# Kernel optimization log

Hardware: AMD Instinct MI355X
Metric: run time of the kernel (lower is better)

Reference implementation:

```python
import jax, jax.numpy as jnp
import numpy as np
from jax import lax

RATE = 2          # self.rate
KS = 3            # kernel_size for matching patches
FUSE_K = 3        # fuse_k
SCALE = 10.0      # softmax_scale
EPS = 1e-4        # NaN guard in l2 norm


def extract_patches(x, size=3, step=1):
    """ZeroPad2d(1) then unfold -> (B, L, C, size, size) with L = Ho*Wo."""
    B, C, H, W = x.shape
    p = lax.conv_general_dilated_patches(
        x, (size, size), (step, step), padding=((1, 1), (1, 1)))
    Ho, Wo = p.shape[2], p.shape[3]
    # feature dim ordering of patches is (C, kh, kw)
    p = p.reshape(B, C, size, size, Ho, Wo)
    return p.transpose(0, 4, 5, 1, 2, 3).reshape(B, Ho * Wo, C, size, size)


def fuse_conv(s):
    """Conv with identity eye(k) kernel, pad 1 (diagonal propagation)."""
    w = jnp.eye(FUSE_K, dtype=s.dtype).reshape(1, 1, FUSE_K, FUSE_K)
    return lax.conv_general_dilated(s, w, (1, 1), ((1, 1), (1, 1)))


def contextual_attention(foreground, background, mask):
    B, C, H, W = foreground.shape
    # raw patches used as deconv filters: (B, L, C, 2*rate, 2*rate)
    raw_w = extract_patches(background, size=2 * RATE, step=RATE)
    # nearest downsample by rate (F.interpolate nearest, scale 1/rate == stride slice)
    fg = foreground[:, :, ::RATE, ::RATE]
    bg = background[:, :, ::RATE, ::RATE]
    fh, fw = fg.shape[2], fg.shape[3]
    bh, bw = bg.shape[2], bg.shape[3]
    # matching patches: (B, L, C, 3, 3), L = bh*bw
    w = extract_patches(bg, KS, 1)
    # mask patches -> per-patch validity (code uses batch 0 of the mask only)
    m = mask[:, :, ::RATE, ::RATE]
    mp = extract_patches(m, KS, 1)[0]            # (L, 1, 3, 3)
    mm = jnp.mean(mp, axis=(1, 2, 3))            # (L,)
    eq = (mm == 0.0).astype(foreground.dtype)[None, :, None, None]  # (1, L, 1, 1)
    # cosine-normalized filters
    norm = jnp.sqrt(jnp.sum(w * w, axis=(2, 3, 4), keepdims=True))
    wn = w / jnp.maximum(norm, EPS)
    # per-batch dynamic conv: scores (B, L, fh, fw)
    def score(f, wi):
        return lax.conv_general_dilated(f[None], wi, (1, 1), ((1, 1), (1, 1)))[0]
    s = jax.vmap(score)(fg, wn)
    # fuse: two identity-kernel convs with raw reshapes (faithful to torch .view,
    # including the discarded second permute in the original code)
    s = s.reshape(B, 1, fh * fw, bh * bw)
    s = fuse_conv(s)
    s = s.reshape(B, fh, fw, bh, bw).transpose(0, 2, 1, 4, 3)
    s = s.reshape(B, 1, fh * fw, bh * bw)
    s = fuse_conv(s)
    s = s.reshape(B, bh * bw, fh, fw)  # raw row-major reinterpret, as torch .view does
    # masked scaled softmax over background-patch dim
    s = s * eq
    s = jax.nn.softmax(s * SCALE, axis=1) * eq
    # per-batch deconv with raw patches as filters (conv_transpose2d stride=rate, pad=1)
    def deconv(si, rwi):
        # torch conv_transpose2d(W:(L,C,4,4)) == dilated conv with flipped, swapped kernel
        wt = jnp.flip(rwi, axis=(-2, -1)).transpose(1, 0, 2, 3)  # (C, L, 4, 4)
        pad = 2 * RATE - 1 - 1  # k - 1 - padding = 2
        return lax.conv_general_dilated(
            si[None], wt, (1, 1), ((pad, pad), (pad, pad)),
            lhs_dilation=(RATE, RATE))[0]
    y = jax.vmap(deconv)(s, raw_w) / 4.0  # (B, C, H, W)
    return y


def setup_inputs() -> dict:
    key = jax.random.key(0)
    k1, k2, k3 = jax.random.split(key, 3)
    B, C, H, W = 8, 128, 64, 64
    foreground = jax.random.normal(k1, (B, C, H, W), jnp.float32)
    background = jax.random.normal(k2, (B, C, H, W), jnp.float32)
    mask = (jax.random.uniform(k3, (1, 1, H, W)) < 0.25).astype(jnp.float32)
    return {"foreground": foreground, "background": background, "mask": mask}


def reference(foreground, background, mask):
    return contextual_attention(foreground, background, mask)
```

## Files before the change

### kernel.cpp

```cpp
#include <hip/hip_runtime.h>

typedef _Float16 half8 __attribute__((ext_vector_type(8)));
typedef float f32x4 __attribute__((ext_vector_type(4)));
typedef unsigned short us8 __attribute__((ext_vector_type(8)));
typedef unsigned short ush;
typedef unsigned int uint32;

#define IMGB 295936u
#define WROW 8704u

#define OFF_FGH  0ull
#define OFF_BGH  2367488ull
#define OFF_BGL  4734976ull
#define OFF_BGT  7102464ull
#define OFF_RN   15491072ull
#define OFF_LIST 15589376ull
#define OFF_NACT 15593472ull
#define OFF_S0   15597568ull
#define OFF_S2   49152000ull
#define OFF_WGT2 82706432ull

static __device__ __forceinline__ ush f2h(float f) {
    union { _Float16 h; ush u; } c; c.h = (_Float16)f; return c.u;
}
static __device__ __forceinline__ float h2f(ush u) {
    union { _Float16 h; ush u; } c; c.u = u; return (float)c.h;
}
__device__ __forceinline__ int untr(int v) { return ((v & 31) << 5) | (v >> 5); }

__global__ void k_prep2(const float* __restrict__ fg, const float* __restrict__ bg,
                        ush* __restrict__ fgh3, ush* __restrict__ bgh,
                        ush* __restrict__ bgl, ush* __restrict__ BGt) {
    int y = blockIdx.x, b = blockIdx.y, t = threadIdx.x;
    __shared__ float lds[64 * 129];
    __shared__ float fls[32 * 129];
    int xx = t & 63;
    for (int c0 = 0; c0 < 128; c0 += 4) {
        int c = c0 + (t >> 6);
        lds[xx * 129 + c] = bg[((b * 128 + c) * 64 + y) * 64 + xx];
    }
    __syncthreads();
    uint32* dst = (uint32*)(BGt + (size_t)(b * 64 + y) * 8192);
    for (int j = t; j < 4096; j += 256) {
        int x = j >> 6, cp = (j & 63) * 2;
        uint32 h0 = f2h(lds[x * 129 + cp]);
        uint32 h1 = f2h(lds[x * 129 + cp + 1]);
        dst[j] = h0 | (h1 << 16);
    }
    if ((y & 1) != 0) return;
    int yd = y >> 1;
    {
        int xq = t & 31, cg = t >> 5;
        for (int c0 = 0; c0 < 128; c0 += 8) {
            int c = c0 + cg;
            fls[xq * 129 + c] = fg[((b * 128 + c) * 64 + y) * 64 + 2 * xq];
        }
    }
    __syncthreads();
    unsigned base = ((b * 34 + yd + 1) * 34 + 1) * 128;
    for (int k = t; k < 2048; k += 256) {
        int x = k >> 6, c = (k & 63) * 2;
        float vb0 = lds[(2 * x) * 129 + c], vb1 = lds[(2 * x) * 129 + c + 1];
        float vf0 = fls[x * 129 + c],       vf1 = fls[x * 129 + c + 1];
        _Float16 bh0 = (_Float16)vb0, bh1 = (_Float16)vb1;
        float br0 = vb0 - (float)bh0, br1 = vb1 - (float)bh1;
        union { _Float16 h; ush u; } x0, x1;
        x0.h = bh0; x1.h = bh1;
        uint32 b01 = (uint32)x0.u | ((uint32)x1.u << 16);
        uint32 l01 = (uint32)f2h(br0) | ((uint32)f2h(br1) << 16);
        ((uint32*)(bgh + base))[k] = b01;
        ((uint32*)(bgl + base))[k] = l01;
        uint32 f01 = (uint32)f2h(vf0) | ((uint32)f2h(vf1) << 16);
        int ch = c >> 6, g = (c >> 3) & 7, cl = c & 7;
        unsigned pix = (unsigned)(yd + 1) * 34 + (x + 1);
        unsigned ui = (((unsigned)(b * 16 + ch * 8 + g) * 1156 + pix) << 2) + (cl >> 1);
        ((uint32*)fgh3)[ui] = f01;
    }
    unsigned cb0 = ((unsigned)(b * 34 + yd + 1) * 34) * 64;
    if (t < 64) {
        ((uint32*)bgh)[cb0 + t] = 0; ((uint32*)bgl)[cb0 + t] = 0;
    } else if (t < 128) {
        unsigned cb1 = cb0 + 33 * 64 + (t - 64);
        ((uint32*)bgh)[cb1] = 0; ((uint32*)bgl)[cb1] = 0;
    } else if (t < 256) {
        int tt = t - 128;
        unsigned pix = (unsigned)(yd + 1) * 34 + ((tt >> 6) ? 33u : 0u);
        int pl = tt & 63, plane = pl >> 2, w = pl & 3;
        ((uint32*)fgh3)[(((unsigned)(b * 16 + plane) * 1156 + pix) << 2) + w] = 0;
    }
    if (yd == 0 || yd == 31) {
        int prow = (yd == 0) ? 0 : 33;
        unsigned rb = (unsigned)(b * 34 + prow) * 2176;
        for (int k = t; k < 2176; k += 256) {
            ((uint32*)bgh)[rb + k] = 0; ((uint32*)bgl)[rb + k] = 0;
            int plane = k / 136, rem = k - plane * 136;
            unsigned pix = (unsigned)prow * 34 + (rem >> 2);
            ((uint32*)fgh3)[(((unsigned)(b * 16 + plane) * 1156 + pix) << 2) + (rem & 3)] = 0;
        }
    }
}

__global__ void k_ssnq(const ush* __restrict__ bgh, const ush* __restrict__ bgl,
                       const float* __restrict__ mask, float* __restrict__ rnorm,
                       int* __restrict__ L, int* __restrict__ nact) {
    int bx = blockIdx.x, b = blockIdx.y, t = threadIdx.x;
    __shared__ float ssh[10][32];
    __shared__ int ps[256];
    if (bx == 4) {
        if (b != 0) return;
        int fl[4], s = 0;
#pragma unroll
        for (int j = 0; j < 4; ++j) {
            int l = t * 4 + j;
            int hm = l >> 5, wm = l & 31;
            int any = 0;
            for (int di = -1; di <= 1; ++di)
                for (int dj = -1; dj <= 1; ++dj) {
                    int yy = hm + di, xxx = wm + dj;
                    if (yy >= 0 && yy < 32 && xxx >= 0 && xxx < 32)
                        any |= (mask[(2 * yy) * 64 + 2 * xxx] != 0.0f);
                }
            fl[j] = !any; s += fl[j];
        }
        ps[t] = s;
        __syncthreads();
        for (int off = 1; off < 256; off <<= 1) {
            int v = (t >= off) ? ps[t - off] : 0;
            __syncthreads();
            ps[t] += v;
            __syncthreads();
        }
        int base = ps[t] - s;
#pragma unroll
        for (int j = 0; j < 4; ++j)
            if (fl[j]) L[base++] = t * 4 + j;
        if (t == 255) nact[0] = ps[255];
        return;
    }
    int r0 = bx * 8;
    for (int idx = t; idx < 320; idx += 256) {
        int row = idx >> 5, xx = idx & 31;
        int gy = r0 - 1 + row;
        float s = 0.f;
        if (gy >= 0 && gy < 32) {
            size_t base = ((size_t)(b * 34 + gy + 1) * 34 + xx + 1) * 128;
            for (int c = 0; c < 128; c += 8) {
                us8 vh = *(const us8*)(bgh + base + c);
                us8 vl = *(const us8*)(bgl + base + c);
#pragma unroll
                for (int j = 0; j < 8; ++j) {
                    float v = h2f(vh[j]) + h2f(vl[j]);
                    s += v * v;
                }
            }
        }
        ssh[row][xx] = s;
    }
    __syncthreads();
    int pr = t >> 5, pc = t & 31;
    float n2 = 0.f;
#pragma unroll
    for (int di = -1; di <= 1; ++di)
#pragma unroll
        for (int dj = -1; dj <= 1; ++dj) {
            int xx = pc + dj;
            if (xx >= 0 && xx < 32) n2 += ssh[pr + 1 + di][xx];
        }
    rnorm[b * 1024 + (r0 + pr) * 32 + pc] = 1.0f / fmaxf(sqrtf(n2), 1e-4f);
}

__global__ __launch_bounds__(256, 2)
void k_smfma(const ush* __restrict__ fgh3, const ush* __restrict__ bgh,
             const ush* __restrict__ bgl, const float* __restrict__ rnorm,
             float* __restrict__ s0) {
    int qt = blockIdx.x, pt = blockIdx.y, b = blockIdx.z;
    int t = threadIdx.x, wid = t >> 6, lane = t & 63;
    int wp = wid >> 1, wq = wid & 1;
    __shared__ ulong2 smem_raw[3328];
    char* smem = (char*)smem_raw;

    const char* base0 = (const char*)bgh + (size_t)b * IMGB + (unsigned)(pt * 4) * WROW;
    const char* base1 = (const char*)bgl + (size_t)b * IMGB + (unsigned)(pt * 4) * WROW;

    f32x4 acc[4][4];
#pragma unroll
    for (int i = 0; i < 4; ++i)
#pragma unroll
        for (int j = 0; j < 4; ++j) acc[i][j] = (f32x4){0.f, 0.f, 0.f, 0.f};

    int r15 = lane & 15, hi2 = lane >> 4;
    for (int ch = 0; ch < 2; ++ch) {
        __syncthreads();
        {
            int pixl = (lane >> 3);
            int sl = lane & 7;
            for (int idx = wid; idx < 52; idx += 4) {
                int a = idx / 26;
                int chunk = idx - a * 26;
                int pix = chunk * 8 + pixl;
                int g = sl ^ (pix & 7);
                const char* sb = a ? base1 : base0;
                const char* gp = sb + ((unsigned)pix << 8) + ((unsigned)ch << 7)
                               + ((unsigned)g << 4);
                char* lp = smem + (unsigned)(a * 26624 + chunk * 1024);
                __builtin_amdgcn_global_load_lds(
                    (const __attribute__((address_space(1))) void*)gp,
                    (__attribute__((address_space(3))) void*)lp, 16, 0, 0);
            }
        }
        __syncthreads();

        const char* Aimg = (const char*)fgh3
                         + (((size_t)(b * 16 + ch * 8)) * 1156 + (unsigned)(qt * 136)) * 16;
        for (int o = 0; o < 9; ++o) {
            int dy = o / 3, dx = o - 3 * (o / 3);
            int pixB[4], pixA[4];
#pragma unroll
            for (int i = 0; i < 4; ++i) {
                pixB[i] = (wp * 2 + (i >> 1) + dy) * 34 + (i & 1) * 16 + r15 + dx;
                pixA[i] = (wq * 2 + (i >> 1) + dy) * 34 + (i & 1) * 16 + r15 + dx;
            }
#pragma unroll
            for (int cc = 0; cc < 2; ++cc) {
                int g = cc * 4 + hi2;
                half8 bh[4], bl[4], af[4];
#pragma unroll
                for (int i = 0; i < 4; ++i) {
                    unsigned offB = ((unsigned)pixB[i] << 7) + ((unsigned)(g ^ (pixB[i] & 7)) << 4);
                    bh[i] = *(const half8*)(smem + offB);
                    bl[i] = *(const half8*)(smem + 26624 + offB);
                    af[i] = *(const half8*)(Aimg + (((size_t)g * 1156 + pixA[i]) << 4));
                }
#pragma unroll
                for (int i = 0; i < 4; ++i)
#pragma unroll
                    for (int j = 0; j < 4; ++j) {
                        acc[i][j] = __builtin_amdgcn_mfma_f32_16x16x32_f16(bh[i], af[j], acc[i][j], 0, 0, 0);
                        acc[i][j] = __builtin_amdgcn_mfma_f32_16x16x32_f16(bl[i], af[j], acc[i][j], 0, 0, 0);
                    }
            }
        }
    }
    int col = lane & 15, rgrp = (lane >> 4) << 2;
#pragma unroll
    for (int i = 0; i < 4; ++i) {
        int Pb = pt * 128 + wp * 64 + i * 16 + rgrp;
        float rn0 = rnorm[b * 1024 + Pb + 0];
        float rn1 = rnorm[b * 1024 + Pb + 1];
        float rn2 = rnorm[b * 1024 + Pb + 2];
        float rn3 = rnorm[b * 1024 + Pb + 3];
#pragma unroll
        for (int j = 0; j < 4; ++j) {
            int Q = qt * 128 + wq * 64 + j * 16 + col;
            float* dst = s0 + ((size_t)(b * 1024 + Pb) << 10) + Q;
            dst[0]    = acc[i][j][0] * rn0;
            dst[1024] = acc[i][j][1] * rn1;
            dst[2048] = acc[i][j][2] * rn2;
            dst[3072] = acc[i][j][3] * rn3;
        }
    }
}

__global__ void k_fuse(const float* __restrict__ s0, float* __restrict__ s2t,
                       const int* __restrict__ L, const int* __restrict__ nactp) {
    int nact = *nactp;
    int b = blockIdx.z;
    int u = blockIdx.x * 256 + threadIdx.x;
    int T = untr(u);
    const float* S = s0 + (size_t)b * 1048576;
    for (int ai = blockIdx.y; ai < nact; ai += 32) {
        int R = L[ai];
        float acc = 0.f;
#pragma unroll
        for (int k = -1; k <= 1; ++k) {
            int Rk = R + k, Tk = T + k;
            if ((unsigned)Rk < 1024u && (unsigned)Tk < 1024u) {
                int Pr = untr(Rk), Qc = untr(Tk);
#pragma unroll
                for (int j = -1; j <= 1; ++j) {
                    int r = Pr + j, cI = Qc + j;
                    if ((unsigned)r < 1024u && (unsigned)cI < 1024u)
                        acc += S[(size_t)r * 1024 + cI];
                }
            }
        }
        s2t[(size_t)b * 1048576 + (size_t)R * 1024 + u] = acc;
    }
}

__global__ __launch_bounds__(256)
void k_ctsw(const ush* __restrict__ BGt, const float* __restrict__ s2t,
            const int* __restrict__ L, const int* __restrict__ nactp,
            ush* __restrict__ CT, ush* __restrict__ W2) {
    int bx = blockIdx.x, b = blockIdx.y, t = threadIdx.x;
    int nact = *nactp;
    __shared__ float sm[32][8], sd[32][8];
    __shared__ float Msh[32], RDsh[32];
    __shared__ ush wt[32][136];
    if (bx < 16) {
        int KPAD = (nact + 31) & ~31;
        int ab = bx, a = ab >> 2, bb = ab & 3;
        for (int ai0 = 0; ai0 < KPAD; ai0 += 256) {
            int ai = ai0 + t;
            if (ai >= KPAD) break;
            int ok = 0;
            const ush* srow = nullptr;
            if (ai < nact) {
                int R = L[ai];
                int hb = R >> 5, wb = R & 31;
                int row = 2 * hb - 1 + a, col = 2 * wb - 1 + bb;
                if (row >= 0 && row < 64 && col >= 0 && col < 64) {
                    ok = 1;
                    srow = BGt + ((size_t)((b * 64 + row) * 64 + col) << 7);
                }
            }
            ush* dst = CT + ((size_t)(b * 16 + ab) << 15) + ai;
#pragma unroll 4
            for (int c = 0; c < 128; ++c)
                dst[(size_t)c << 8] = ok ? srow[c] : (ush)0;
        }
        return;
    }
    int uc = bx - 16;
    int u0 = uc * 32;
    int part = t >> 5, ul = t & 31;
    {
        const float* S = s2t + (size_t)b * 1048576 + u0 + ul;
        float m = -3e38f, d = 0.f;
        for (int ai = part; ai < nact; ai += 8) {
            float v = S[(size_t)L[ai] << 10];
            if (v > m) { d *= expf(10.f * (m - v)); m = v; }
            d += expf(10.f * (v - m));
        }
        sm[ul][part] = m; sd[ul][part] = d;
    }
    __syncthreads();
    if (t < 32) {
        float mm = -3e38f, dd = 0.f;
#pragma unroll
        for (int p = 0; p < 8; ++p) {
            float m2 = sm[t][p], d2 = sd[t][p];
            if (m2 > mm) { dd *= expf(10.f * (mm - m2)); mm = m2; dd += d2; }
            else dd += d2 * expf(10.f * (m2 - mm));
        }
        int cnt0 = 1024 - nact;
        if (cnt0 > 0) {
            if (mm < 0.f) { dd *= expf(10.f * mm); mm = 0.f; }
            dd += (float)cnt0 * expf(-10.f * mm);
        }
        Msh[t] = mm; RDsh[t] = 1.f / dd;
    }
    __syncthreads();
    for (int kp = 0; kp < 16; ++kp) {
        int k = kp * 8 + part;
        float w = 0.f;
        if (k < nact) {
            float v = s2t[((size_t)(b * 1024 + L[k]) << 10) + u0 + ul];
            w = expf(10.f * (v - Msh[ul])) * RDsh[ul];
        }
        wt[ul][k] = f2h(w);
    }
    __syncthreads();
    {
        int ur = t >> 3, kb = t & 7;
        int uu = u0 + ur;
        int p1 = (uu & 31) + 1, q1 = (uu >> 5) + 1;
        ush* dstr = W2 + (((size_t)(b * 35 + p1) * 35 + q1) << 7) + kb * 16;
        *(half8*)dstr       = *(const half8*)&wt[ur][kb * 16];
        *(half8*)(dstr + 8) = *(const half8*)&wt[ur][kb * 16 + 8];
    }
    for (int r = uc; r < 1225; r += 32) {
        int p1 = r / 35, q1 = r - p1 * 35;
        if (p1 < 1 || p1 > 32 || q1 < 1 || q1 > 32) {
            uint32* row = (uint32*)(W2 + (((size_t)(b * 35 + p1) * 35 + q1) << 7));
            if (t < 64) row[t] = 0;
        }
    }
}

__global__ __launch_bounds__(256, 4)
void k_dgemm(const ush* __restrict__ CT, const ush* __restrict__ W2,
             const int* __restrict__ nactp, float* __restrict__ y) {
    int nact = *nactp;
    int KPAD = (nact + 31) & ~31;
    int pt2 = blockIdx.x;
    int par = blockIdx.y, b = blockIdx.z;
    int a_lo = par >> 1, b_lo = par & 1;
    int P0 = 1 - a_lo, Q0 = 1 - b_lo;
    int p_lo = P0 + pt2;
    int wid = threadIdx.x >> 6, lane = threadIdx.x & 63;
    int r15 = lane & 15, kg = (lane >> 4) << 3;

    f32x4 acc[2][2];
#pragma unroll
    for (int i = 0; i < 2; ++i)
#pragma unroll
        for (int j = 0; j < 2; ++j) acc[i][j] = (f32x4){0.f, 0.f, 0.f, 0.f};

    for (int k0 = 0; k0 < KPAD; k0 += 32) {
#pragma unroll
        for (int pp = 0; pp < 2; ++pp)
#pragma unroll
            for (int qq = 0; qq < 2; ++qq) {
                int ab = (a_lo + 2 * pp) * 4 + (b_lo + 2 * qq);
                const ush* Ab = CT + ((size_t)(b * 16 + ab) << 15)
                              + ((unsigned)(wid * 32) << 8) + k0 + kg;
                int p1 = p_lo - pp + 1;
                int q1b = Q0 - qq + 1;
                const ush* Bb = W2 + (((size_t)(b * 35 + p1) * 35 + q1b) << 7) + k0 + kg;
                half8 A[2], B[2];
                A[0] = *(const half8*)(Ab + ((unsigned)r15 << 8));
                A[1] = *(const half8*)(Ab + ((unsigned)(16 + r15) << 8));
                B[0] = *(const half8*)(Bb + ((unsigned)r15 << 7));
                B[1] = *(const half8*)(Bb + ((unsigned)(16 + r15) << 7));
#pragma unroll
                for (int i = 0; i < 2; ++i)
#pragma unroll
                    for (int j = 0; j < 2; ++j)
                        acc[i][j] = __builtin_amdgcn_mfma_f32_16x16x32_f16(A[i], B[j], acc[i][j], 0, 0, 0);
            }
    }
    int col = r15, rgrp = (lane >> 4) << 2;
    int oy = 2 * p_lo + a_lo - 1;
#pragma unroll
    for (int i = 0; i < 2; ++i) {
        int c = wid * 32 + i * 16 + rgrp;
#pragma unroll
        for (int j = 0; j < 2; ++j) {
            int q_lo = Q0 + j * 16 + col;
            int ox = 2 * q_lo + b_lo - 1;
            float* Y = y + ((size_t)((b * 128 + c) * 64 + oy) << 6) + ox;
            Y[0]         = acc[i][j][0] * 0.25f;
            Y[4096]      = acc[i][j][1] * 0.25f;
            Y[2 * 4096]  = acc[i][j][2] * 0.25f;
            Y[3 * 4096]  = acc[i][j][3] * 0.25f;
        }
    }
}

extern "C" void kernel_launch(void* const* d_in, const int* in_sizes, int n_in,
                              void* d_out, int out_size, void* d_ws, size_t ws_size,
                              hipStream_t stream) {
    (void)in_sizes; (void)n_in; (void)out_size; (void)ws_size;
    const float* fg   = (const float*)d_in[0];
    const float* bg   = (const float*)d_in[1];
    const float* mask = (const float*)d_in[2];
    float* y = (float*)d_out;
    char* ws = (char*)d_ws;

    ush*   fgh3  = (ush*)(ws + OFF_FGH);
    ush*   bgh   = (ush*)(ws + OFF_BGH);
    ush*   bgl   = (ush*)(ws + OFF_BGL);
    ush*   BGt   = (ush*)(ws + OFF_BGT);
    float* rnorm = (float*)(ws + OFF_RN);
    int*   Lst   = (int*)(ws + OFF_LIST);
    int*   nact  = (int*)(ws + OFF_NACT);
    float* s0    = (float*)(ws + OFF_S0);
    ush*   CT    = (ush*)(ws + OFF_S0);
    float* s2t   = (float*)(ws + OFF_S2);
    ush*   W2    = (ush*)(ws + OFF_WGT2);

    k_prep2<<<dim3(64, 8), 256, 0, stream>>>(fg, bg, fgh3, bgh, bgl, BGt);
    k_ssnq<<<dim3(5, 8), 256, 0, stream>>>(bgh, bgl, mask, rnorm, Lst, nact);
    k_smfma<<<dim3(8, 8, 8), 256, 0, stream>>>(fgh3, bgh, bgl, rnorm, s0);
    k_fuse<<<dim3(4, 32, 8), 256, 0, stream>>>(s0, s2t, Lst, nact);
    k_ctsw<<<dim3(48, 8), 256, 0, stream>>>(BGt, s2t, Lst, nact, CT, W2);
    k_dgemm<<<dim3(32, 4, 8), 256, 0, stream>>>(CT, W2, nact, y);
}
```

Baseline: 116.3 us.

## Fold norm/mask kernel into prep and compute patch norms inside score GEMM

Removes the separate k_ssnq launch. The per-pixel channel sum of squares is now computed in k_prep2 from the fp32 background already staged in LDS, and an extra block handles the mask scan. k_smfma then builds each 3x3 patch's reciprocal norm from those sums into shared memory before its GEMM. This saves one kernel launch and a reread of the split-half background, at the cost of a little redundant stencil work per GEMM block. Norms now come from exact fp32 values instead of the hi+lo half reconstruction.

```diff
diff --git a/kernel.cpp b/kernel.cpp
--- a/kernel.cpp
+++ b/kernel.cpp
@@ -13,7 +13,7 @@
 #define OFF_BGH  2367488ull
 #define OFF_BGL  4734976ull
 #define OFF_BGT  7102464ull
-#define OFF_RN   15491072ull
+#define OFF_SS   15523840ull
 #define OFF_LIST 15589376ull
 #define OFF_NACT 15593472ull
 #define OFF_S0   15597568ull
@@ -29,11 +29,47 @@
 __device__ __forceinline__ int untr(int v) { return ((v & 31) << 5) | (v >> 5); }
 
 __global__ void k_prep2(const float* __restrict__ fg, const float* __restrict__ bg,
+                        const float* __restrict__ mask,
                         ush* __restrict__ fgh3, ush* __restrict__ bgh,
-                        ush* __restrict__ bgl, ush* __restrict__ BGt) {
+                        ush* __restrict__ bgl, ush* __restrict__ BGt,
+                        float* __restrict__ SS, int* __restrict__ L,
+                        int* __restrict__ nact) {
     int y = blockIdx.x, b = blockIdx.y, t = threadIdx.x;
     __shared__ float lds[64 * 129];
     __shared__ float fls[32 * 129];
+    __shared__ float sm2[32][8];
+    __shared__ int ps[256];
+    if (y == 64) {
+        if (b != 0) return;
+        int fl[4], s = 0;
+#pragma unroll
+        for (int j = 0; j < 4; ++j) {
+            int l = t * 4 + j;
+            int hm = l >> 5, wm = l & 31;
+            int any = 0;
+            for (int di = -1; di <= 1; ++di)
+                for (int dj = -1; dj <= 1; ++dj) {
+                    int yy = hm + di, xxx = wm + dj;
+                    if (yy >= 0 && yy < 32 && xxx >= 0 && xxx < 32)
+                        any |= (mask[(2 * yy) * 64 + 2 * xxx] != 0.0f);
+                }
+            fl[j] = !any; s += fl[j];
+        }
+        ps[t] = s;
+        __syncthreads();
+        for (int off = 1; off < 256; off <<= 1) {
+            int v = (t >= off) ? ps[t - off] : 0;
+            __syncthreads();
+            ps[t] += v;
+            __syncthreads();
+        }
+        int base = ps[t] - s;
+#pragma unroll
+        for (int j = 0; j < 4; ++j)
+            if (fl[j]) L[base++] = t * 4 + j;
+        if (t == 255) nact[0] = ps[255];
+        return;
+    }
     int xx = t & 63;
     for (int c0 = 0; c0 < 128; c0 += 4) {
         int c = c0 + (t >> 6);
@@ -56,7 +92,24 @@
             fls[xq * 129 + c] = fg[((b * 128 + c) * 64 + y) * 64 + 2 * xq];
         }
     }
+    {
+        int xd = t & 31, part = t >> 5;
+        float s = 0.f;
+        int c0 = part * 16;
+#pragma unroll
+        for (int c = 0; c < 16; ++c) {
+            float v = lds[(2 * xd) * 129 + c0 + c];
+            s += v * v;
+        }
+        sm2[xd][part] = s;
+    }
     __syncthreads();
+    if (t < 32) {
+        float s = 0.f;
+#pragma unroll
+        for (int p = 0; p < 8; ++p) s += sm2[t][p];
+        SS[b * 1024 + yd * 32 + t] = s;
+    }
     unsigned base = ((b * 34 + yd + 1) * 34 + 1) * 128;
     for (int k = t; k < 2048; k += 256) {
         int x = k >> 6, c = (k & 63) * 2;
@@ -100,84 +153,34 @@
     }
 }
 
-__global__ void k_ssnq(const ush* __restrict__ bgh, const ush* __restrict__ bgl,
-                       const float* __restrict__ mask, float* __restrict__ rnorm,
-                       int* __restrict__ L, int* __restrict__ nact) {
-    int bx = blockIdx.x, b = blockIdx.y, t = threadIdx.x;
-    __shared__ float ssh[10][32];
-    __shared__ int ps[256];
-    if (bx == 4) {
-        if (b != 0) return;
-        int fl[4], s = 0;
-#pragma unroll
-        for (int j = 0; j < 4; ++j) {
-            int l = t * 4 + j;
-            int hm = l >> 5, wm = l & 31;
-            int any = 0;
-            for (int di = -1; di <= 1; ++di)
-                for (int dj = -1; dj <= 1; ++dj) {
-                    int yy = hm + di, xxx = wm + dj;
-                    if (yy >= 0 && yy < 32 && xxx >= 0 && xxx < 32)
-                        any |= (mask[(2 * yy) * 64 + 2 * xxx] != 0.0f);
-                }
-            fl[j] = !any; s += fl[j];
-        }
-        ps[t] = s;
-        __syncthreads();
-        for (int off = 1; off < 256; off <<= 1) {
-            int v = (t >= off) ? ps[t - off] : 0;
-            __syncthreads();
-            ps[t] += v;
-            __syncthreads();
-        }
-        int base = ps[t] - s;
-#pragma unroll
-        for (int j = 0; j < 4; ++j)
-            if (fl[j]) L[base++] = t * 4 + j;
-        if (t == 255) nact[0] = ps[255];
-        return;
-    }
-    int r0 = bx * 8;
-    for (int idx = t; idx < 320; idx += 256) {
-        int row = idx >> 5, xx = idx & 31;
-        int gy = r0 - 1 + row;
-        float s = 0.f;
-        if (gy >= 0 && gy < 32) {
-            size_t base = ((size_t)(b * 34 + gy + 1) * 34 + xx + 1) * 128;
-            for (int c = 0; c < 128; c += 8) {
-                us8 vh = *(const us8*)(bgh + base + c);
-                us8 vl = *(const us8*)(bgl + base + c);
-#pragma unroll
-                for (int j = 0; j < 8; ++j) {
-                    float v = h2f(vh[j]) + h2f(vl[j]);
-                    s += v * v;
-                }
-            }
-        }
-        ssh[row][xx] = s;
-    }
-    __syncthreads();
-    int pr = t >> 5, pc = t & 31;
-    float n2 = 0.f;
-#pragma unroll
-    for (int di = -1; di <= 1; ++di)
-#pragma unroll
-        for (int dj = -1; dj <= 1; ++dj) {
-            int xx = pc + dj;
-            if (xx >= 0 && xx < 32) n2 += ssh[pr + 1 + di][xx];
-        }
-    rnorm[b * 1024 + (r0 + pr) * 32 + pc] = 1.0f / fmaxf(sqrtf(n2), 1e-4f);
-}
-
 __global__ __launch_bounds__(256, 2)
 void k_smfma(const ush* __restrict__ fgh3, const ush* __restrict__ bgh,
-             const ush* __restrict__ bgl, const float* __restrict__ rnorm,
+             const ush* __restrict__ bgl, const float* __restrict__ SS,
              float* __restrict__ s0) {
     int qt = blockIdx.x, pt = blockIdx.y, b = blockIdx.z;
     int t = threadIdx.x, wid = t >> 6, lane = t & 63;
     int wp = wid >> 1, wq = wid & 1;
     __shared__ ulong2 smem_raw[3328];
+    __shared__ float rnl[128];
     char* smem = (char*)smem_raw;
+
+    if (t < 128) {
+        int pr = (pt << 2) + (t >> 5), pc = t & 31;
+        float n2 = 0.f;
+#pragma unroll
+        for (int di = -1; di <= 1; ++di) {
+            int r = pr + di;
+            if ((unsigned)r < 32u) {
+                const float* Srow = SS + b * 1024 + r * 32;
+#pragma unroll
+                for (int dj = -1; dj <= 1; ++dj) {
+                    int c2 = pc + dj;
+                    if ((unsigned)c2 < 32u) n2 += Srow[c2];
+                }
+            }
+        }
+        rnl[t] = 1.0f / fmaxf(sqrtf(n2), 1e-4f);
+    }
 
     const char* base0 = (const char*)bgh + (size_t)b * IMGB + (unsigned)(pt * 4) * WROW;
     const char* base1 = (const char*)bgl + (size_t)b * IMGB + (unsigned)(pt * 4) * WROW;
@@ -244,11 +247,12 @@
     int col = lane & 15, rgrp = (lane >> 4) << 2;
 #pragma unroll
     for (int i = 0; i < 4; ++i) {
-        int Pb = pt * 128 + wp * 64 + i * 16 + rgrp;
-        float rn0 = rnorm[b * 1024 + Pb + 0];
-        float rn1 = rnorm[b * 1024 + Pb + 1];
-        float rn2 = rnorm[b * 1024 + Pb + 2];
-        float rn3 = rnorm[b * 1024 + Pb + 3];
+        int Pl = wp * 64 + i * 16 + rgrp;
+        int Pb = pt * 128 + Pl;
+        float rn0 = rnl[Pl + 0];
+        float rn1 = rnl[Pl + 1];
+        float rn2 = rnl[Pl + 2];
+        float rn3 = rnl[Pl + 3];
 #pragma unroll
         for (int j = 0; j < 4; ++j) {
             int Q = qt * 128 + wq * 64 + j * 16 + col;
@@ -452,7 +456,7 @@
     ush*   bgh   = (ush*)(ws + OFF_BGH);
     ush*   bgl   = (ush*)(ws + OFF_BGL);
     ush*   BGt   = (ush*)(ws + OFF_BGT);
-    float* rnorm = (float*)(ws + OFF_RN);
+    float* SS    = (float*)(ws + OFF_SS);
     int*   Lst   = (int*)(ws + OFF_LIST);
     int*   nact  = (int*)(ws + OFF_NACT);
     float* s0    = (float*)(ws + OFF_S0);
@@ -460,9 +464,8 @@
     float* s2t   = (float*)(ws + OFF_S2);
     ush*   W2    = (ush*)(ws + OFF_WGT2);
 
-    k_prep2<<<dim3(64, 8), 256, 0, stream>>>(fg, bg, fgh3, bgh, bgl, BGt);
-    k_ssnq<<<dim3(5, 8), 256, 0, stream>>>(bgh, bgl, mask, rnorm, Lst, nact);
-    k_smfma<<<dim3(8, 8, 8), 256, 0, stream>>>(fgh3, bgh, bgl, rnorm, s0);
+    k_prep2<<<dim3(65, 8), 256, 0, stream>>>(fg, bg, mask, fgh3, bgh, bgl, BGt, SS, Lst, nact);
+    k_smfma<<<dim3(8, 8, 8), 256, 0, stream>>>(fgh3, bgh, bgl, SS, s0);
     k_fuse<<<dim3(4, 32, 8), 256, 0, stream>>>(s0, s2t, Lst, nact);
     k_ctsw<<<dim3(48, 8), 256, 0, stream>>>(BGt, s2t, Lst, nact, CT, W2);
     k_dgemm<<<dim3(32, 4, 8), 256, 0, stream>>>(CT, W2, nact, y);
```

New measurement: 108.9 us, median of 3. 6.3% less time.
